# Kernel optimization log

Hardware: AMD Instinct MI355X
Metric: run time of the kernel (lower is better)

The kernel has to match this reference:

```python
import jax, jax.numpy as jnp
import numpy as np

N, E, F_IN = 50000, 800000, 128
H1, C1 = 4, 32          # layer 1: heads, channels (concat -> 128)
H2, C2 = 1, 40          # layer 2: out heads, num_class (mean over heads)
NEG_SLOPE = 0.2


def setup_inputs() -> dict:
    key = jax.random.key(0)
    ks = jax.random.split(key, 10)
    x = jax.random.normal(ks[0], (N, F_IN), dtype=jnp.float32)
    edge_index = jax.random.randint(ks[1], (2, E), 0, N, dtype=jnp.int32)
    s1 = 1.0 / np.sqrt(F_IN)
    s2 = 1.0 / np.sqrt(H1 * C1)
    W1 = jax.random.normal(ks[2], (F_IN, H1 * C1), dtype=jnp.float32) * s1
    att_src1 = jax.random.normal(ks[3], (H1, C1), dtype=jnp.float32) * s1
    att_dst1 = jax.random.normal(ks[4], (H1, C1), dtype=jnp.float32) * s1
    b1 = jnp.zeros((H1 * C1,), dtype=jnp.float32)
    W2 = jax.random.normal(ks[5], (H1 * C1, H2 * C2), dtype=jnp.float32) * s2
    att_src2 = jax.random.normal(ks[6], (H2, C2), dtype=jnp.float32) * s2
    att_dst2 = jax.random.normal(ks[7], (H2, C2), dtype=jnp.float32) * s2
    b2 = jnp.zeros((C2,), dtype=jnp.float32)
    return {"x": x, "edge_index": edge_index, "W1": W1, "att_src1": att_src1,
            "att_dst1": att_dst1, "b1": b1, "W2": W2, "att_src2": att_src2,
            "att_dst2": att_dst2, "b2": b2}


def _gat_layer(x, src, dst, W, a_src, a_dst, b, concat):
    # PyG GATConv (eval): linear -> per-head attention logits on edges ->
    # segment-softmax over each destination's in-edges -> scatter-aggregate.
    n = x.shape[0]
    Hh, C = a_src.shape
    h = (x @ W).reshape(n, Hh, C)                       # [N,H,C]
    al_s = jnp.sum(h * a_src, axis=-1)                  # [N,H]
    al_d = jnp.sum(h * a_dst, axis=-1)                  # [N,H]
    alpha = jax.nn.leaky_relu(al_s[src] + al_d[dst], NEG_SLOPE)  # [E,H]
    m = jax.lax.stop_gradient(jax.ops.segment_max(alpha, dst, num_segments=n))
    e = jnp.exp(alpha - m[dst])
    denom = jax.ops.segment_sum(e, dst, num_segments=n)
    a = e / (denom[dst] + 1e-16)                        # [E,H]
    out = jax.ops.segment_sum(h[src] * a[..., None], dst, num_segments=n)
    out = out.reshape(n, Hh * C) if concat else out.mean(axis=1)
    return out + b


def reference(x, edge_index, W1, att_src1, att_dst1, b1, W2, att_src2, att_dst2, b2):
    n = x.shape[0]
    loop = jnp.arange(n, dtype=edge_index.dtype)        # GATConv add_self_loops=True
    src = jnp.concatenate([edge_index[0], loop])
    dst = jnp.concatenate([edge_index[1], loop])
    h = _gat_layer(x, src, dst, W1, att_src1, att_dst1, b1, concat=True)
    h = jax.nn.elu(h)
    out = _gat_layer(h, src, dst, W2, att_src2, att_dst2, b2, concat=False)
    return out
```

## Files before the change

kernel.cpp:

```cpp
#include <hip/hip_runtime.h>
#include <hip/hip_bf16.h>
#include <hip/hip_fp16.h>
#include <math.h>

constexpr int N_NODES = 50000;
constexpr int E_EDGES = 800000;
constexpr float NEG_SLOPE = 0.2f;
constexpr int CAP = 64;

typedef _Float16 half8 __attribute__((ext_vector_type(8)));
typedef _Float16 half2v __attribute__((ext_vector_type(2)));
typedef float    floatx4 __attribute__((ext_vector_type(4)));

static inline int cdiv(long long a, int b) { return (int)((a + b - 1) / b); }

__device__ inline float leaky(float a) { return a > 0.f ? a : NEG_SLOPE * a; }
__device__ inline unsigned pack2h(float a, float b) {
    union { _Float16 h[2]; unsigned u; } p;
    p.h[0] = (_Float16)a; p.h[1] = (_Float16)b; return p.u;
}
__device__ inline float2 unp2h(unsigned u) {
    __half2 hh = *reinterpret_cast<__half2*>(&u);
    return __half22float2(hh);
}
__device__ inline float sel4(const float4& v, int h) {
    float a = (h & 2) ? v.z : v.x;
    float b = (h & 2) ? v.w : v.y;
    return (h & 1) ? b : a;
}

__global__ __launch_bounds__(256) void gemm1_kernel(const float* __restrict__ x,
                                                    const float* __restrict__ W,
                                                    const float* __restrict__ as1,
                                                    const float* __restrict__ ad1,
                                                    unsigned short* __restrict__ h1h,
                                                    float* __restrict__ als,
                                                    float* __restrict__ ald) {
    __shared__ _Float16 xS[64 * 136];
    __shared__ _Float16 wtS[128 * 136];
    __shared__ float asld[128], adld[128];
    int t = threadIdx.x;
    int row0 = blockIdx.x * 64;
    if (t < 128) { asld[t] = as1[t]; adld[t] = ad1[t]; }
    #pragma unroll
    for (int i = 0; i < 8; ++i) {
        int fi = i * 256 + t;
        int r = fi >> 5, c4 = (fi & 31) * 4;
        int gr = row0 + r;
        float4 v = make_float4(0.f, 0.f, 0.f, 0.f);
        if (gr < N_NODES) v = *(const float4*)&x[(size_t)gr * 128 + c4];
        union { _Float16 h[4]; uint2 u; } pk;
        pk.h[0] = (_Float16)v.x; pk.h[1] = (_Float16)v.y;
        pk.h[2] = (_Float16)v.z; pk.h[3] = (_Float16)v.w;
        *(uint2*)&xS[r * 136 + c4] = pk.u;
    }
    #pragma unroll
    for (int i = 0; i < 8; ++i) {
        int fi = i * 256 + t;
        int kp = fi & 63, nq = fi >> 6;
        float4 va = *(const float4*)&W[(size_t)(2 * kp) * 128 + nq * 4];
        float4 vb = *(const float4*)&W[(size_t)(2 * kp + 1) * 128 + nq * 4];
        *(unsigned*)&wtS[(nq * 4 + 0) * 136 + 2 * kp] = pack2h(va.x, vb.x);
        *(unsigned*)&wtS[(nq * 4 + 1) * 136 + 2 * kp] = pack2h(va.y, vb.y);
        *(unsigned*)&wtS[(nq * 4 + 2) * 136 + 2 * kp] = pack2h(va.z, vb.z);
        *(unsigned*)&wtS[(nq * 4 + 3) * 136 + 2 * kp] = pack2h(va.w, vb.w);
    }
    __syncthreads();

    int w = t >> 6, lane = t & 63, quad = lane >> 4, l16 = lane & 15;
    floatx4 z = {0.f, 0.f, 0.f, 0.f};
    floatx4 c[4][2];
    #pragma unroll
    for (int rt = 0; rt < 4; ++rt) { c[rt][0] = z; c[rt][1] = z; }
    #pragma unroll
    for (int ks = 0; ks < 4; ++ks) {
        int ko = ks * 32 + quad * 8;
        half8 b0 = *(const half8*)&wtS[(w * 32 + l16) * 136 + ko];
        half8 b1 = *(const half8*)&wtS[(w * 32 + 16 + l16) * 136 + ko];
        #pragma unroll
        for (int rt = 0; rt < 4; ++rt) {
            half8 a = *(const half8*)&xS[(rt * 16 + l16) * 136 + ko];
            c[rt][0] = __builtin_amdgcn_mfma_f32_16x16x32_f16(a, b0, c[rt][0], 0, 0, 0);
            c[rt][1] = __builtin_amdgcn_mfma_f32_16x16x32_f16(a, b1, c[rt][1], 0, 0, 0);
        }
    }
    __syncthreads();
    #pragma unroll
    for (int rt = 0; rt < 4; ++rt)
        #pragma unroll
        for (int ctl = 0; ctl < 2; ++ctl)
            #pragma unroll
            for (int reg = 0; reg < 4; ++reg)
                xS[(rt * 16 + quad * 4 + reg) * 136 + (w * 32 + ctl * 16 + l16)]
                    = (_Float16)c[rt][ctl][reg];
    __syncthreads();
    int r = t >> 2, hq = t & 3;
    int n = row0 + r;
    if (n < N_NODES) {
        float ps = 0.f, pd = 0.f;
        #pragma unroll
        for (int i = 0; i < 4; ++i) {
            uint4 uv = *(uint4*)&xS[r * 136 + hq * 32 + i * 8];
            *(uint4*)&h1h[(size_t)n * 128 + hq * 32 + i * 8] = uv;
            union { uint4 u; _Float16 h[8]; } cv; cv.u = uv;
            #pragma unroll
            for (int k = 0; k < 8; ++k) {
                float v = (float)cv.h[k];
                ps += v * asld[hq * 32 + i * 8 + k];
                pd += v * adld[hq * 32 + i * 8 + k];
            }
        }
        als[n * 4 + hq] = ps;
        ald[n * 4 + hq] = pd;
    }
}

__global__ __launch_bounds__(256) void link_kernel(const int* __restrict__ ei,
                                                   int* __restrict__ head,
                                                   int2* __restrict__ next2) {
    int e = blockIdx.x * 256 + threadIdx.x;
    if (e >= E_EDGES) return;
    int s = ei[e], d = ei[E_EDGES + e];
    int old = atomicExch(&head[d], e);
    next2[e] = make_int2(s, old);
}

__global__ __launch_bounds__(256) void traverse_fixed_kernel(const int* __restrict__ head,
                                                             const int2* __restrict__ next2,
                                                             unsigned short* __restrict__ csr16,
                                                             int* __restrict__ deg) {
    int d = blockIdx.x * 256 + threadIdx.x;
    if (d >= N_NODES) return;
    int base = d * CAP;
    csr16[base] = (unsigned short)d;
    int c = 1;
    int e = head[d];
    while (e >= 0 && c < CAP) {
        int2 v = next2[e];
        csr16[base + c] = (unsigned short)v.x;
        e = v.y;
        ++c;
    }
    deg[d] = c;
}

__global__ __launch_bounds__(256) void agg1_kernel(const int* __restrict__ deg_,
                                                   const unsigned short* __restrict__ csr16,
                                                   const float4* __restrict__ als4,
                                                   const float4* __restrict__ ald4,
                                                   const unsigned short* __restrict__ h1h,
                                                   const float* __restrict__ b1,
                                                   unsigned short* __restrict__ out1h) {
    int wv   = threadIdx.x >> 6;
    int lane = threadIdx.x & 63;
    int half = lane >> 5;
    int l    = lane & 31;
    int d    = blockIdx.x * 4 + wv;
    int dg   = deg_[d];
    int base = d * CAP;
    float4 aldd = ald4[d];
    int head = l >> 3;
    float d_h = sel4(aldd, head);

    float sm = 0.f;
    float acc[4] = {0.f, 0.f, 0.f, 0.f};
    int sfirst = (int)csr16[base];
    for (int j = 0; j < dg; j += 16) {
        uint4 blkA = *(const uint4*)&csr16[base + j];
        uint4 blkB = *(const uint4*)&csr16[base + j + 8];
        unsigned bw[8] = { blkA.x, blkA.y, blkA.z, blkA.w,
                           blkB.x, blkB.y, blkB.z, blkB.w };
        int ss[8];
        #pragma unroll
        for (int p = 0; p < 8; ++p) {
            unsigned b = __builtin_amdgcn_readfirstlane(bw[p]);
            int e0 = (int)(b & 0xffff), e1 = (int)(b >> 16);
            int mys = half ? e1 : e0;
            if (j + 2 * p + half >= dg) mys = sfirst;
            ss[p] = mys;
        }
        uint2 hv[8];
        #pragma unroll
        for (int p = 0; p < 8; ++p)
            hv[p] = *(const uint2*)(h1h + ((size_t)ss[p] << 7) + 4 * l);
        float ww[8];
        #pragma unroll
        for (int p = 0; p < 8; ++p) {
            float4 a = als4[ss[p]];
            float w = __expf(leaky(sel4(a, head) + d_h));
            ww[p] = (j + 2 * p + half < dg) ? w : 0.f;
            sm += ww[p];
        }
        half2v hacc0 = { (_Float16)0.f, (_Float16)0.f };
        half2v hacc1 = { (_Float16)0.f, (_Float16)0.f };
        #pragma unroll
        for (int p = 0; p < 8; ++p) {
            half2v v0 = *reinterpret_cast<half2v*>(&hv[p].x);
            half2v v1 = *reinterpret_cast<half2v*>(&hv[p].y);
            _Float16 hw = (_Float16)ww[p];
            half2v hwv = { hw, hw };
            hacc0 += v0 * hwv;
            hacc1 += v1 * hwv;
        }
        acc[0] += (float)hacc0[0]; acc[1] += (float)hacc0[1];
        acc[2] += (float)hacc1[0]; acc[3] += (float)hacc1[1];
    }
    sm += __shfl_xor(sm, 32);
    #pragma unroll
    for (int k = 0; k < 4; ++k) acc[k] += __shfl_xor(acc[k], 32);
    if (half == 0) {
        float inv = 1.f / (sm + 1e-16f);
        float v[4];
        #pragma unroll
        for (int k = 0; k < 4; ++k) {
            v[k] = acc[k] * inv + b1[4 * l + k];
            v[k] = v[k] > 0.f ? v[k] : __expf(v[k]) - 1.f;
        }
        uint2 o;
        o.x = pack2h(v[0], v[1]);
        o.y = pack2h(v[2], v[3]);
        *(uint2*)&out1h[(size_t)d * 128 + 4 * l] = o;
    }
}

__global__ __launch_bounds__(256) void gemm2_kernel(const unsigned short* __restrict__ out1h,
                                                    const float* __restrict__ W2,
                                                    const float* __restrict__ as2,
                                                    const float* __restrict__ ad2,
                                                    unsigned short* __restrict__ h2h,
                                                    float* __restrict__ als,
                                                    float* __restrict__ ald) {
    __shared__ _Float16 aS[64 * 136];
    __shared__ _Float16 wt2[48 * 136];
    __shared__ float asld[40], adld[40];
    int t = threadIdx.x;
    int row0 = blockIdx.x * 64;
    if (t < 40) { asld[t] = as2[t]; adld[t] = ad2[t]; }
    #pragma unroll
    for (int i = 0; i < 4; ++i) {
        int fi = i * 256 + t;
        int r = fi >> 4, s8 = (fi & 15) * 8;
        int gr = row0 + r;
        uint4 v = make_uint4(0u, 0u, 0u, 0u);
        if (gr < N_NODES) v = *(const uint4*)&out1h[(size_t)gr * 128 + s8];
        *(uint4*)&aS[r * 136 + s8] = v;
    }
    #pragma unroll
    for (int i = 0; i < 3; ++i) {
        int fi = i * 256 + t;
        if (fi < 640) {
            int kp = fi & 63, nq = fi >> 6;
            float4 va = *(const float4*)&W2[(size_t)(2 * kp) * 40 + nq * 4];
            float4 vb = *(const float4*)&W2[(size_t)(2 * kp + 1) * 40 + nq * 4];
            *(unsigned*)&wt2[(nq * 4 + 0) * 136 + 2 * kp] = pack2h(va.x, vb.x);
            *(unsigned*)&wt2[(nq * 4 + 1) * 136 + 2 * kp] = pack2h(va.y, vb.y);
            *(unsigned*)&wt2[(nq * 4 + 2) * 136 + 2 * kp] = pack2h(va.z, vb.z);
            *(unsigned*)&wt2[(nq * 4 + 3) * 136 + 2 * kp] = pack2h(va.w, vb.w);
        }
    }
    __syncthreads();

    int w = t >> 6, lane = t & 63, quad = lane >> 4, l16 = lane & 15;
    floatx4 z = {0.f, 0.f, 0.f, 0.f};
    floatx4 c0 = z, c1 = z, c2 = z;
    #pragma unroll
    for (int ks = 0; ks < 4; ++ks) {
        int ko = ks * 32 + quad * 8;
        half8 a  = *(const half8*)&aS[(w * 16 + l16) * 136 + ko];
        half8 b0 = *(const half8*)&wt2[(l16) * 136 + ko];
        half8 b1 = *(const half8*)&wt2[(16 + l16) * 136 + ko];
        half8 b2 = *(const half8*)&wt2[(32 + l16) * 136 + ko];
        c0 = __builtin_amdgcn_mfma_f32_16x16x32_f16(a, b0, c0, 0, 0, 0);
        c1 = __builtin_amdgcn_mfma_f32_16x16x32_f16(a, b1, c1, 0, 0, 0);
        c2 = __builtin_amdgcn_mfma_f32_16x16x32_f16(a, b2, c2, 0, 0, 0);
    }
    __syncthreads();
    #pragma unroll
    for (int reg = 0; reg < 4; ++reg) {
        int rr = (w * 16 + quad * 4 + reg) * 136;
        aS[rr + l16]      = (_Float16)c0[reg];
        aS[rr + 16 + l16] = (_Float16)c1[reg];
        aS[rr + 32 + l16] = (_Float16)c2[reg];
    }
    __syncthreads();
    for (int fi = t; fi < 320; fi += 256) {
        int r = fi / 5, s = fi - r * 5;
        int n = row0 + r;
        if (n < N_NODES) {
            uint4 v = *(uint4*)&aS[r * 136 + s * 8];
            *(uint4*)&h2h[(size_t)n * 40 + s * 8] = v;
        }
    }
    int r = t >> 2, q = t & 3;
    int n = row0 + r;
    float ps = 0.f, pd = 0.f;
    #pragma unroll
    for (int i = 0; i < 10; ++i) {
        int cc = q * 10 + i;
        float v = (float)aS[r * 136 + cc];
        ps += v * asld[cc]; pd += v * adld[cc];
    }
    ps += __shfl_xor(ps, 1); ps += __shfl_xor(ps, 2);
    pd += __shfl_xor(pd, 1); pd += __shfl_xor(pd, 2);
    if (q == 0 && n < N_NODES) { als[n] = ps; ald[n] = pd; }
}

__global__ __launch_bounds__(256) void agg2_kernel(const int* __restrict__ deg_,
                                                   const unsigned short* __restrict__ csr16,
                                                   const float* __restrict__ als,
                                                   const float* __restrict__ ald,
                                                   const unsigned short* __restrict__ h2h,
                                                   const float* __restrict__ b2,
                                                   float* __restrict__ out) {
    int wv   = threadIdx.x >> 6;
    int lane = threadIdx.x & 63;
    int d    = blockIdx.x * 4 + wv;
    int dg   = deg_[d];
    int base = d * CAP;
    float aldd = ald[d];

    int slot = lane / 20;
    int idx  = lane - slot * 20;
    int sfirst = (int)csr16[base];
    float sm = 0.f, acc0 = 0.f, acc1 = 0.f;
    if (lane < 60) {
        for (int jb = 0; jb < dg; jb += 12) {
            int ss[4]; unsigned hv[4]; float ww[4];
            #pragma unroll
            for (int i = 0; i < 4; ++i) {
                int jj = jb + slot + 3 * i;
                ss[i] = (jj < dg) ? (int)csr16[base + jj] : sfirst;
            }
            #pragma unroll
            for (int i = 0; i < 4; ++i)
                hv[i] = *(const unsigned*)(h2h + (size_t)ss[i] * 40 + 2 * idx);
            #pragma unroll
            for (int i = 0; i < 4; ++i) {
                int jj = jb + slot + 3 * i;
                float w = __expf(leaky(als[ss[i]] + aldd));
                ww[i] = (jj < dg) ? w : 0.f;
            }
            #pragma unroll
            for (int i = 0; i < 4; ++i) {
                float2 f = unp2h(hv[i]);
                acc0 += f.x * ww[i]; acc1 += f.y * ww[i]; sm += ww[i];
            }
        }
    }
    float s1 = __shfl(sm,   idx + 20), s2 = __shfl(sm,   idx + 40);
    float t0 = __shfl(acc0, idx + 20), t1 = __shfl(acc0, idx + 40);
    float u0 = __shfl(acc1, idx + 20), u1 = __shfl(acc1, idx + 40);
    sm += s1 + s2; acc0 += t0 + t1; acc1 += u0 + u1;
    if (lane < 20) {
        float inv = 1.f / (sm + 1e-16f);
        float2 o = make_float2(acc0 * inv + b2[2 * lane], acc1 * inv + b2[2 * lane + 1]);
        *(float2*)&out[(size_t)d * 40 + 2 * lane] = o;
    }
}

constexpr size_t OFF_H1H    = 0;
constexpr size_t OFF_OUT1   = 3200000;
constexpr size_t OFF_ALS1   = 6400000;
constexpr size_t OFF_ALD1   = 6600000;
constexpr size_t OFF_HEAD   = 6800000;
constexpr size_t OFF_DEG    = 6860000;
constexpr size_t OFF_CSRF   = 6920000;
constexpr size_t WS_FLOATS  = 8520000;

extern "C" void kernel_launch(void* const* d_in, const int* in_sizes, int n_in,
                              void* d_out, int out_size, void* d_ws, size_t ws_size,
                              hipStream_t stream) {
    const float* x   = (const float*)d_in[0];
    const int*   ei  = (const int*)  d_in[1];
    const float* W1  = (const float*)d_in[2];
    const float* as1 = (const float*)d_in[3];
    const float* ad1 = (const float*)d_in[4];
    const float* b1  = (const float*)d_in[5];
    const float* W2  = (const float*)d_in[6];
    const float* as2 = (const float*)d_in[7];
    const float* ad2 = (const float*)d_in[8];
    const float* b2  = (const float*)d_in[9];
    float* out = (float*)d_out;

    if (ws_size < WS_FLOATS * sizeof(float)) return;

    float* ws = (float*)d_ws;
    unsigned short* h1h   = (unsigned short*)(ws + OFF_H1H);
    unsigned short* h2h   = (unsigned short*)(ws + OFF_H1H);
    int2*  next2   = (int2*)(ws + OFF_H1H);
    unsigned short* out1h = (unsigned short*)(ws + OFF_OUT1);
    float* als1    = ws + OFF_ALS1;
    float* ald1    = ws + OFF_ALD1;
    float* als2    = ws + OFF_ALS1;
    float* ald2    = ws + OFF_ALD1;
    int*   head    = (int*)(ws + OFF_HEAD);
    int*   deg     = (int*)(ws + OFF_DEG);
    unsigned short* csr16 = (unsigned short*)(ws + OFF_CSRF);

    int ngrid = cdiv(N_NODES, 256);

    hipMemsetAsync(head, 0xFF, (size_t)N_NODES * sizeof(int), stream);
    link_kernel<<<cdiv(E_EDGES, 256), 256, 0, stream>>>(ei, head, next2);
    traverse_fixed_kernel<<<ngrid, 256, 0, stream>>>(head, next2, csr16, deg);

    gemm1_kernel<<<cdiv(N_NODES, 64), 256, 0, stream>>>(x, W1, as1, ad1, h1h, als1, ald1);
    agg1_kernel<<<N_NODES / 4, 256, 0, stream>>>(deg, csr16,
                                                 (const float4*)als1, (const float4*)ald1,
                                                 h1h, b1, out1h);

    gemm2_kernel<<<cdiv(N_NODES, 64), 256, 0, stream>>>(out1h, W2, as2, ad2, h2h, als2, ald2);
    agg2_kernel<<<N_NODES / 4, 256, 0, stream>>>(deg, csr16, als2, ald2, h2h, b2, out);
}
```

Baseline: 238.0 us.

## Fuse edge-link pass into gemm1 launch and share attention weights via shuffles

The edge linked-list construction now runs as extra blocks inside the gemm1 launch, so the two independent stages overlap in one grid and one launch is removed. The next2 buffer moves to its own workspace region so it no longer aliases h1h. In agg1, each lane computes one edge-head attention weight, reading a scalar als per lane, and the weights are distributed with shuffles. This replaces the redundant float4 gathers and exp computations that were repeated across lanes. The cost is a larger workspace and heavier LDS allocation for the link blocks, which may reduce their occupancy.

New measurement: 226.7 us. -4.7%, faster.

```diff
diff --git a/kernel.cpp b/kernel.cpp
--- a/kernel.cpp
+++ b/kernel.cpp
@@ -7,6 +7,8 @@
 constexpr int E_EDGES = 800000;
 constexpr float NEG_SLOPE = 0.2f;
 constexpr int CAP = 64;
+constexpr int G1_BLOCKS   = (N_NODES + 63) / 64;
+constexpr int LINK_BLOCKS = (E_EDGES + 255) / 256;
 
 typedef _Float16 half8 __attribute__((ext_vector_type(8)));
 typedef _Float16 half2v __attribute__((ext_vector_type(2)));
@@ -29,17 +31,31 @@
     return (h & 1) ? b : a;
 }
 
-__global__ __launch_bounds__(256) void gemm1_kernel(const float* __restrict__ x,
-                                                    const float* __restrict__ W,
-                                                    const float* __restrict__ as1,
-                                                    const float* __restrict__ ad1,
-                                                    unsigned short* __restrict__ h1h,
-                                                    float* __restrict__ als,
-                                                    float* __restrict__ ald) {
+__global__ __launch_bounds__(256) void gemm1_link_kernel(const float* __restrict__ x,
+                                                         const float* __restrict__ W,
+                                                         const float* __restrict__ as1,
+                                                         const float* __restrict__ ad1,
+                                                         unsigned short* __restrict__ h1h,
+                                                         float* __restrict__ als,
+                                                         float* __restrict__ ald,
+                                                         const int* __restrict__ ei,
+                                                         int* __restrict__ head_,
+                                                         int2* __restrict__ next2) {
     __shared__ _Float16 xS[64 * 136];
     __shared__ _Float16 wtS[128 * 136];
     __shared__ float asld[128], adld[128];
     int t = threadIdx.x;
+
+    if (blockIdx.x >= G1_BLOCKS) {
+        int e = (blockIdx.x - G1_BLOCKS) * 256 + t;
+        if (e < E_EDGES) {
+            int s = ei[e], d = ei[E_EDGES + e];
+            int old = atomicExch(&head_[d], e);
+            next2[e] = make_int2(s, old);
+        }
+        return;
+    }
+
     int row0 = blockIdx.x * 64;
     if (t < 128) { asld[t] = as1[t]; adld[t] = ad1[t]; }
     #pragma unroll
@@ -113,16 +129,6 @@
         als[n * 4 + hq] = ps;
         ald[n * 4 + hq] = pd;
     }
-}
-
-__global__ __launch_bounds__(256) void link_kernel(const int* __restrict__ ei,
-                                                   int* __restrict__ head,
-                                                   int2* __restrict__ next2) {
-    int e = blockIdx.x * 256 + threadIdx.x;
-    if (e >= E_EDGES) return;
-    int s = ei[e], d = ei[E_EDGES + e];
-    int old = atomicExch(&head[d], e);
-    next2[e] = make_int2(s, old);
 }
 
 __global__ __launch_bounds__(256) void traverse_fixed_kernel(const int* __restrict__ head,
@@ -146,7 +152,7 @@
 
 __global__ __launch_bounds__(256) void agg1_kernel(const int* __restrict__ deg_,
                                                    const unsigned short* __restrict__ csr16,
-                                                   const float4* __restrict__ als4,
+                                                   const float* __restrict__ als,
                                                    const float4* __restrict__ ald4,
                                                    const unsigned short* __restrict__ h1h,
                                                    const float* __restrict__ b1,
@@ -155,17 +161,22 @@
     int lane = threadIdx.x & 63;
     int half = lane >> 5;
     int l    = lane & 31;
+    int myhead = l >> 3;
+    int we   = lane & 15;
+    int wh   = lane >> 4;
     int d    = blockIdx.x * 4 + wv;
     int dg   = deg_[d];
     int base = d * CAP;
     float4 aldd = ald4[d];
-    int head = l >> 3;
-    float d_h = sel4(aldd, head);
+    float d_hw = sel4(aldd, wh);
 
     float sm = 0.f;
     float acc[4] = {0.f, 0.f, 0.f, 0.f};
     int sfirst = (int)csr16[base];
     for (int j = 0; j < dg; j += 16) {
+        int s_w = (int)csr16[base + j + we];
+        float av = als[s_w * 4 + wh];
+        float wgt = (j + we < dg) ? __expf(leaky(av + d_hw)) : 0.f;
         uint4 blkA = *(const uint4*)&csr16[base + j];
         uint4 blkB = *(const uint4*)&csr16[base + j + 8];
         unsigned bw[8] = { blkA.x, blkA.y, blkA.z, blkA.w,
@@ -186,9 +197,7 @@
         float ww[8];
         #pragma unroll
         for (int p = 0; p < 8; ++p) {
-            float4 a = als4[ss[p]];
-            float w = __expf(leaky(sel4(a, head) + d_h));
-            ww[p] = (j + 2 * p + half < dg) ? w : 0.f;
+            ww[p] = __shfl(wgt, 16 * myhead + 2 * p + half);
             sm += ww[p];
         }
         half2v hacc0 = { (_Float16)0.f, (_Float16)0.f };
@@ -365,7 +374,8 @@
 constexpr size_t OFF_HEAD   = 6800000;
 constexpr size_t OFF_DEG    = 6860000;
 constexpr size_t OFF_CSRF   = 6920000;
-constexpr size_t WS_FLOATS  = 8520000;
+constexpr size_t OFF_NEXT2  = 8520000;
+constexpr size_t WS_FLOATS  = 10120000;
 
 extern "C" void kernel_launch(void* const* d_in, const int* in_sizes, int n_in,
                               void* d_out, int out_size, void* d_ws, size_t ws_size,
@@ -387,7 +397,6 @@
     float* ws = (float*)d_ws;
     unsigned short* h1h   = (unsigned short*)(ws + OFF_H1H);
     unsigned short* h2h   = (unsigned short*)(ws + OFF_H1H);
-    int2*  next2   = (int2*)(ws + OFF_H1H);
     unsigned short* out1h = (unsigned short*)(ws + OFF_OUT1);
     float* als1    = ws + OFF_ALS1;
     float* ald1    = ws + OFF_ALD1;
@@ -396,16 +405,17 @@
     int*   head    = (int*)(ws + OFF_HEAD);
     int*   deg     = (int*)(ws + OFF_DEG);
     unsigned short* csr16 = (unsigned short*)(ws + OFF_CSRF);
+    int2*  next2   = (int2*)(ws + OFF_NEXT2);
 
     int ngrid = cdiv(N_NODES, 256);
 
     hipMemsetAsync(head, 0xFF, (size_t)N_NODES * sizeof(int), stream);
-    link_kernel<<<cdiv(E_EDGES, 256), 256, 0, stream>>>(ei, head, next2);
+    gemm1_link_kernel<<<G1_BLOCKS + LINK_BLOCKS, 256, 0, stream>>>(
+        x, W1, as1, ad1, h1h, als1, ald1, ei, head, next2);
     traverse_fixed_kernel<<<ngrid, 256, 0, stream>>>(head, next2, csr16, deg);
 
-    gemm1_kernel<<<cdiv(N_NODES, 64), 256, 0, stream>>>(x, W1, as1, ad1, h1h, als1, ald1);
-    agg1_kernel<<<N_NODES / 4, 256, 0, stream>>>(deg, csr16,
-                                                 (const float4*)als1, (const float4*)ald1,
+    agg1_kernel<<<N_NODES / 4, 256, 0, stream>>>(deg, csr16, als1,
+                                                 (const float4*)ald1,
                                                  h1h, b1, out1h);
 
     gemm2_kernel<<<cdiv(N_NODES, 64), 256, 0, stream>>>(out1h, W2, as2, ad2, h2h, als2, ald2);
```
